# Performance work log

Hardware: AMD Instinct MI355X
Metric: run time of the kernel (lower is better)

## Reference

```python
import jax, jax.numpy as jnp
import numpy as np

B = 4096          # number of sampled constraints (batch)
H = 1024          # hidden_size
N_UNIT = 5
MAXD = 4          # max(DEPTHS)
TAU = 1.0
N_STEPS = N_UNIT * (1 + 2 * MAXD)  # 45
CLIST = np.linspace(10.0, 20.0, 5).astype(np.float32)
NSC = 11
DEPTH_VALS = np.array([2, 3, 4])
RATIO_VALS = np.array([3, 4, 6])
KS_VALS = np.array([3, 5, 7])


def setup_inputs() -> dict:
    key = jax.random.key(0)
    ks = jax.random.split(key, 20)
    def p(k, shape):
        return jax.random.uniform(k, shape, minval=-0.1, maxval=0.1, dtype=jnp.float32)
    return {
        'constraints': jax.random.uniform(ks[0], (B,), minval=10.0, maxval=20.0, dtype=jnp.float32),
        'superclass_id': 3,
        'gumbel_u': jax.random.uniform(ks[1], (N_STEPS, B, 3), minval=1e-6, maxval=1.0 - 1e-6, dtype=jnp.float32),
        'cond_emb': p(ks[2], (len(CLIST), H // 2)),
        'sc_emb': p(ks[3], (NSC, H // 2)),
        'depth_emb': p(ks[4], (3, H)),
        'ratio_emb': p(ks[5], (3, H)),
        'ks_emb': p(ks[6], (3, H)),
        'W_ih': p(ks[7], (4 * H, H)), 'b_ih': p(ks[8], (4 * H,)),
        'W_hh': p(ks[9], (4 * H, H)), 'b_hh': p(ks[10], (4 * H,)),
        'depth_W': p(ks[11], (3, H)), 'depth_b': p(ks[12], (3,)),
        'width_W': p(ks[13], (3, H)), 'width_b': p(ks[14], (3,)),
        'ks_W': p(ks[15], (3, H)), 'ks_b': p(ks[16], (3,)),
    }


def reference(constraints, superclass_id, gumbel_u, cond_emb, sc_emb, depth_emb, ratio_emb,
              ks_emb, W_ih, b_ih, W_hh, b_hh, depth_W, depth_b, width_W, width_b, ks_W, ks_b):
    clist = jnp.asarray(CLIST)
    # linear_interpolation: find bracketing interval for each constraint
    idx = jnp.clip(jnp.searchsorted(clist, constraints, side='right') - 1, 0, clist.shape[0] - 2)
    left, right = clist[idx], clist[idx + 1]
    w = ((right - constraints) / (right - left))[:, None]
    cemb = w * cond_emb[idx] + (1.0 - w) * cond_emb[idx + 1]          # [B, H/2]
    sce = jnp.broadcast_to(sc_emb[superclass_id], (constraints.shape[0], sc_emb.shape[1]))
    embed = jnp.concatenate([cemb, sce], axis=1)                       # [B, H]
    h = jnp.zeros((constraints.shape[0], H), embed.dtype)
    c = h

    def lstm(x, h, c):
        gates = x @ W_ih.T + b_ih + h @ W_hh.T + b_hh                  # [B, 4H]
        i, f, g, o = jnp.split(gates, 4, axis=-1)
        c2 = jax.nn.sigmoid(f) * c + jax.nn.sigmoid(i) * jnp.tanh(g)
        h2 = jax.nn.sigmoid(o) * jnp.tanh(c2)
        return h2, c2

    def gsample(logits, u):
        g = -jnp.log(-jnp.log(u))
        y_soft = jax.nn.softmax((logits + g) / TAU, axis=-1)
        onehot = jax.nn.one_hot(jnp.argmax(y_soft, -1), logits.shape[-1], dtype=y_soft.dtype)
        y_hard = onehot - jax.lax.stop_gradient(y_soft) + y_soft       # straight-through
        return jnp.argmax(y_hard, -1), y_soft, y_hard

    t = 0
    d_idx, d_probs, d_wbs = [], [], []
    r_idx, r_probs, r_wbs = [], [], []
    k_idx, k_probs, k_wbs = [], [], []
    for _unit in range(N_UNIT):
        h, c = lstm(embed, h, c)
        s, ys, yh = gsample(h @ depth_W.T + depth_b, gumbel_u[t]); t += 1
        d_idx.append(s); d_probs.append(ys); d_wbs.append(yh)
        embed = depth_emb[s]
        for _blk in range(MAXD):
            h, c = lstm(embed, h, c)
            s, ys, yh = gsample(h @ width_W.T + width_b, gumbel_u[t]); t += 1
            r_idx.append(s); r_probs.append(ys); r_wbs.append(yh)
            embed = ratio_emb[s]
            h, c = lstm(embed, h, c)
            s, ys, yh = gsample(h @ ks_W.T + ks_b, gumbel_u[t]); t += 1
            k_idx.append(s); k_probs.append(ys); k_wbs.append(yh)
            embed = ks_emb[s]

    depths = jnp.asarray(DEPTH_VALS)[jnp.stack(d_idx)]   # [5, B]
    ratios = jnp.asarray(RATIO_VALS)[jnp.stack(r_idx)]   # [20, B]
    kss = jnp.asarray(KS_VALS)[jnp.stack(k_idx)]         # [20, B]
    return (depths, ratios, kss,
            jnp.stack(d_wbs), jnp.stack(d_probs),
            jnp.stack(r_wbs), jnp.stack(r_probs),
            jnp.stack(k_wbs), jnp.stack(k_probs))
```

## Files before the change

kernel.cpp:

```cpp
#include <hip/hip_runtime.h>
#include <cmath>

namespace {

typedef _Float16 f16;
typedef f16 f16x8 __attribute__((ext_vector_type(8)));
typedef f16 f16x4 __attribute__((ext_vector_type(4)));
typedef float f32x4 __attribute__((ext_vector_type(4)));

constexpr int B  = 4096;
constexpr int H  = 1024;
constexpr int FH = 4 * H;
constexpr int NSTEPS = 45;
constexpr float INVS = 1.0f / 2048.0f;

__device__ __forceinline__ float sigf(float x) { return 1.0f / (1.0f + expf(-x)); }

struct HL { f16 h, l; };
__device__ __forceinline__ HL split16(float a) {
  float ah = (float)(f16)a;
  if (fabsf(a) < 6.1035156e-5f) ah = 0.0f;
  HL r; r.h = (f16)ah; r.l = (f16)((a - ah) * 2048.0f); return r;
}

__device__ __forceinline__ void async16(f16* lds_dst, const f16* gsrc) {
  __builtin_amdgcn_global_load_lds(
      (const __attribute__((address_space(1))) void*)gsrc,
      (__attribute__((address_space(3))) void*)lds_dst, 16, 0, 0);
}

__global__ void convertW_kernel(const float* __restrict__ W,
                                f16* __restrict__ Whi, f16* __restrict__ Wlo) {
  size_t i = ((size_t)blockIdx.x * 256 + threadIdx.x) * 4;
  float4 v = *(const float4*)(W + i);
  HL a = split16(v.x), b = split16(v.y), c = split16(v.z), d = split16(v.w);
  f16x4 hi = {a.h, b.h, c.h, d.h};
  f16x4 lo = {a.l, b.l, c.l, d.l};
  *(f16x4*)(Whi + i) = hi;
  *(f16x4*)(Wlo + i) = lo;
}

__global__ void precompute_kernel(
    const float* __restrict__ W_ih, const float* __restrict__ b_ih, const float* __restrict__ b_hh,
    const float* __restrict__ depth_emb, const float* __restrict__ ratio_emb, const float* __restrict__ ks_emb,
    const float* __restrict__ cond_emb, const float* __restrict__ sc_emb, const int* __restrict__ sid_p,
    float* __restrict__ tblD, float* __restrict__ tblR, float* __restrict__ tblK,
    float* __restrict__ condp, float* __restrict__ base0) {
  const int w4   = threadIdx.x >> 6;
  const int lane = threadIdx.x & 63;
  const int j    = blockIdx.x * 4 + w4;
  const float* wr = W_ih + (size_t)j * H;
  const int k = lane * 16;
  float4 wv0 = *(const float4*)(wr + k);
  float4 wv1 = *(const float4*)(wr + k + 4);
  float4 wv2 = *(const float4*)(wr + k + 8);
  float4 wv3 = *(const float4*)(wr + k + 12);

  auto dot = [&](const float* e) -> float {
    float4 e0 = *(const float4*)(e);
    float4 e1 = *(const float4*)(e + 4);
    float4 e2 = *(const float4*)(e + 8);
    float4 e3 = *(const float4*)(e + 12);
    return e0.x*wv0.x + e0.y*wv0.y + e0.z*wv0.z + e0.w*wv0.w
         + e1.x*wv1.x + e1.y*wv1.y + e1.z*wv1.z + e1.w*wv1.w
         + e2.x*wv2.x + e2.y*wv2.y + e2.z*wv2.z + e2.w*wv2.w
         + e3.x*wv3.x + e3.y*wv3.y + e3.z*wv3.z + e3.w*wv3.w;
  };

  float a[15];
  a[0] = dot(depth_emb + k);       a[1] = dot(depth_emb + H + k);   a[2] = dot(depth_emb + 2*H + k);
  a[3] = dot(ratio_emb + k);       a[4] = dot(ratio_emb + H + k);   a[5] = dot(ratio_emb + 2*H + k);
  a[6] = dot(ks_emb + k);          a[7] = dot(ks_emb + H + k);      a[8] = dot(ks_emb + 2*H + k);
  a[9] = a[10] = a[11] = a[12] = a[13] = a[14] = 0.0f;
  constexpr int HH = H / 2;
  int sid = sid_p[0];
  if (lane < 32) {
    a[9]  = dot(cond_emb + 0*HH + k);
    a[10] = dot(cond_emb + 1*HH + k);
    a[11] = dot(cond_emb + 2*HH + k);
    a[12] = dot(cond_emb + 3*HH + k);
    a[13] = dot(cond_emb + 4*HH + k);
  } else {
    a[14] = dot(sc_emb + sid*HH + (k - HH));
  }
  #pragma unroll
  for (int i = 0; i < 15; ++i) {
    #pragma unroll
    for (int off = 32; off > 0; off >>= 1) a[i] += __shfl_xor(a[i], off);
  }
  if (lane == 0) {
    float bias = b_ih[j] + b_hh[j];
    tblD[0*FH+j]=a[0]+bias; tblD[1*FH+j]=a[1]+bias; tblD[2*FH+j]=a[2]+bias;
    tblR[0*FH+j]=a[3]+bias; tblR[1*FH+j]=a[4]+bias; tblR[2*FH+j]=a[5]+bias;
    tblK[0*FH+j]=a[6]+bias; tblK[1*FH+j]=a[7]+bias; tblK[2*FH+j]=a[8]+bias;
    condp[0*FH+j]=a[9]; condp[1*FH+j]=a[10]; condp[2*FH+j]=a[11];
    condp[3*FH+j]=a[12]; condp[4*FH+j]=a[13];
    base0[j] = a[14] + bias;
  }
}

__global__ void step0_kernel(const float* __restrict__ constraints,
                             const float* __restrict__ condp, const float* __restrict__ base0,
                             f16* __restrict__ hhi, f16* __restrict__ hlo, float* __restrict__ c) {
  int idx = blockIdx.x * blockDim.x + threadIdx.x;
  int b = idx >> 10;
  int j = idx & (H - 1);
  float cv = constraints[b];
  int i0 = 0;
  if (cv >= 12.5f) i0 = 1;
  if (cv >= 15.0f) i0 = 2;
  if (cv >= 17.5f) i0 = 3;
  float right = 10.0f + 2.5f * (float)(i0 + 1);
  float w = (right - cv) / 2.5f;
  const float* c0 = condp + (size_t)i0 * FH;
  const float* c1 = c0 + FH;
  float iw = 1.0f - w;
  float xi = w*c0[j]       + iw*c1[j]       + base0[j];
  float xg = w*c0[2*H+j]   + iw*c1[2*H+j]   + base0[2*H+j];
  float xo = w*c0[3*H+j]   + iw*c1[3*H+j]   + base0[3*H+j];
  float cn = sigf(xi) * tanhf(xg);
  float hn = sigf(xo) * tanhf(cn);
  c[idx] = cn;
  HL s = split16(hn);
  hhi[idx] = s.h; hlo[idx] = s.l;
}

constexpr int BUFE = 24576;

__global__ __launch_bounds__(512, 2) void lstm_step_mfma(
    const f16* __restrict__ hhi, const f16* __restrict__ hlo,
    f16* __restrict__ nhhi, f16* __restrict__ nhlo,
    float* __restrict__ cbuf,
    const f16* __restrict__ Whi, const f16* __restrict__ Wlo,
    const float* __restrict__ tbl, const int* __restrict__ sel) {
  __shared__ __align__(16) f16 lds[3 * BUFE];

  const int tid  = threadIdx.x;
  const int lane = tid & 63;
  const int w    = tid >> 6;
  const int wm   = w >> 1, wn = w & 1;
  const int l15  = lane & 15;
  const int kq   = lane >> 4;

  const int L   = blockIdx.x;
  const int xcd = L & 7, seq = L >> 3;
  const int jb  = (xcd << 2) + (seq & 3);
  const int bb  = seq >> 2;
  const int b0  = bb << 8;
  const int j0  = jb << 5;

  f32x4 accH[4][4] = {};
  f32x4 accL[4][4] = {};

  int offA[4], offB[4];
  #pragma unroll
  for (int mf = 0; mf < 4; ++mf) {
    int R = wm * 64 + mf * 16 + l15;
    int c = kq ^ (R & 3) ^ ((R >> 2) & 3);
    offA[mf] = R * 32 + c * 8;
  }
  #pragma unroll
  for (int nf = 0; nf < 4; ++nf) {
    int R = nf * 32 + wn * 16 + l15;
    int c = kq ^ (R & 3) ^ ((R >> 2) & 3);
    offB[nf] = 16384 + R * 32 + c * 8;
  }

  const int rs = tid >> 2, cs = tid & 3;
  const int r1 = 128 + rs;
  const int cl0 = cs ^ (rs & 3) ^ ((rs >> 2) & 3);
  const int cl1 = cs ^ (r1 & 3) ^ ((r1 >> 2) & 3);
  const int wrow = ((rs >> 5) << 10) + j0 + (rs & 31);
  const f16* sA0h = hhi + (size_t)(b0 + rs) * H + cl0 * 8;
  const f16* sA0l = hlo + (size_t)(b0 + rs) * H + cl0 * 8;
  const f16* sA1h = hhi + (size_t)(b0 + r1) * H + cl1 * 8;
  const f16* sA1l = hlo + (size_t)(b0 + r1) * H + cl1 * 8;
  const f16* sBh  = Whi + (size_t)wrow * H + cl0 * 8;
  const f16* sBl  = Wlo + (size_t)wrow * H + cl0 * 8;
  const int dA0 = w * 512, dA1 = 4096 + w * 512, dB = 16384 + w * 512;

  auto stage6 = [&](f16* buf, int ko) {
    async16(buf + dA0,        sA0h + ko);
    async16(buf + dA0 + 8192, sA0l + ko);
    async16(buf + dA1,        sA1h + ko);
    async16(buf + dA1 + 8192, sA1l + ko);
    async16(buf + dB,         sBh + ko);
    async16(buf + dB + 4096,  sBl + ko);
  };

  f16 *bA = lds, *bB = lds + BUFE, *bC = lds + 2 * BUFE;

  f16x8 bhX[4], bhY[4];

  stage6(bA, 0);
  stage6(bB, 32);
  asm volatile("s_waitcnt vmcnt(0)" ::: "memory");
  __builtin_amdgcn_s_barrier();
  #pragma unroll
  for (int nf = 0; nf < 4; ++nf) bhX[nf] = *(const f16x8*)(bA + offB[nf]);

  auto tile = [&](int kt, f16x8 (&bhC)[4], f16x8 (&bhN)[4]) {
    if (kt < 30) stage6(bC, (kt + 2) * 32);

    f16x8 ah[4], al[4], bl[4];
    #pragma unroll
    for (int mf = 0; mf < 4; ++mf) ah[mf] = *(const f16x8*)(bA + offA[mf]);
    #pragma unroll
    for (int mf = 0; mf < 4; ++mf) al[mf] = *(const f16x8*)(bA + offA[mf] + 8192);
    #pragma unroll
    for (int nf = 0; nf < 4; ++nf) bl[nf] = *(const f16x8*)(bA + offB[nf] + 4096);
    if (kt < 31) {
      #pragma unroll
      for (int nf = 0; nf < 4; ++nf) bhN[nf] = *(const f16x8*)(bB + offB[nf]);
    }

    #pragma unroll
    for (int mf = 0; mf < 4; ++mf)
      #pragma unroll
      for (int nf = 0; nf < 4; ++nf)
        accH[mf][nf] = __builtin_amdgcn_mfma_f32_16x16x32_f16(ah[mf], bhC[nf], accH[mf][nf], 0, 0, 0);
    #pragma unroll
    for (int mf = 0; mf < 4; ++mf)
      #pragma unroll
      for (int nf = 0; nf < 4; ++nf)
        accL[mf][nf] = __builtin_amdgcn_mfma_f32_16x16x32_f16(ah[mf], bl[nf], accL[mf][nf], 0, 0, 0);
    #pragma unroll
    for (int mf = 0; mf < 4; ++mf)
      #pragma unroll
      for (int nf = 0; nf < 4; ++nf)
        accL[mf][nf] = __builtin_amdgcn_mfma_f32_16x16x32_f16(al[mf], bhC[nf], accL[mf][nf], 0, 0, 0);

    asm volatile("s_waitcnt vmcnt(0)" ::: "memory");
    __builtin_amdgcn_s_barrier();
    f16* t = bA; bA = bB; bB = bC; bC = t;
  };

  for (int kt = 0; kt < 32; kt += 2) {
    tile(kt,     bhX, bhY);
    tile(kt + 1, bhY, bhX);
  }

  const int j = j0 + wn * 16 + l15;
  #pragma unroll
  for (int mf = 0; mf < 4; ++mf) {
    #pragma unroll
    for (int r = 0; r < 4; ++r) {
      int b = b0 + wm * 64 + mf * 16 + kq * 4 + r;
      int s = sel[b];
      const float* tb = tbl + (size_t)s * FH + j;
      float gi = accH[mf][0][r] + accL[mf][0][r] * INVS + tb[0];
      float gf = accH[mf][1][r] + accL[mf][1][r] * INVS + tb[H];
      float gg = accH[mf][2][r] + accL[mf][2][r] * INVS + tb[2*H];
      float go = accH[mf][3][r] + accL[mf][3][r] * INVS + tb[3*H];
      size_t off = (size_t)b * H + j;
      float cp = cbuf[off];
      float cn = sigf(gf) * cp + sigf(gi) * tanhf(gg);
      float hn = sigf(go) * tanhf(cn);
      cbuf[off] = cn;
      HL sp = split16(hn);
      nhhi[off] = sp.h;
      nhlo[off] = sp.l;
    }
  }
}

__global__ void sampler_kernel(const f16* __restrict__ hhi, const f16* __restrict__ hlo,
                               const float* __restrict__ selW, const float* __restrict__ selb,
                               const float* __restrict__ gu,
                               float* __restrict__ val_out, float* __restrict__ wb_out,
                               float* __restrict__ p_out,
                               float v0, float v1, float v2,
                               int* __restrict__ sel) {
  int wave = threadIdx.x >> 6;
  int lane = threadIdx.x & 63;
  int b = blockIdx.x * 4 + wave;
  const f16* hh = hhi + (size_t)b * H;
  const f16* hl = hlo + (size_t)b * H;
  float acc0 = 0, acc1 = 0, acc2 = 0;
  #pragma unroll
  for (int ch = 0; ch < 4; ++ch) {
    int k = ch * 256 + lane * 4;
    f16x4 vh = *(const f16x4*)(hh + k);
    f16x4 vl = *(const f16x4*)(hl + k);
    float x0 = (float)vh[0] + (float)vl[0] * INVS;
    float x1 = (float)vh[1] + (float)vl[1] * INVS;
    float x2 = (float)vh[2] + (float)vl[2] * INVS;
    float x3 = (float)vh[3] + (float)vl[3] * INVS;
    float4 w0 = *(const float4*)(selW + k);
    float4 w1 = *(const float4*)(selW + H + k);
    float4 w2 = *(const float4*)(selW + 2*H + k);
    acc0 += x0*w0.x + x1*w0.y + x2*w0.z + x3*w0.w;
    acc1 += x0*w1.x + x1*w1.y + x2*w1.z + x3*w1.w;
    acc2 += x0*w2.x + x1*w2.y + x2*w2.z + x3*w2.w;
  }
  #pragma unroll
  for (int off = 32; off > 0; off >>= 1) {
    acc0 += __shfl_xor(acc0, off);
    acc1 += __shfl_xor(acc1, off);
    acc2 += __shfl_xor(acc2, off);
  }
  if (lane == 0) {
    float y0 = acc0 + selb[0] - logf(-logf(gu[(size_t)b*3 + 0]));
    float y1 = acc1 + selb[1] - logf(-logf(gu[(size_t)b*3 + 1]));
    float y2 = acc2 + selb[2] - logf(-logf(gu[(size_t)b*3 + 2]));
    int s = 0;
    float best = y0;
    if (y1 > best) { s = 1; best = y1; }
    if (y2 > best) { s = 2; best = y2; }
    float e0 = expf(y0 - best), e1 = expf(y1 - best), e2 = expf(y2 - best);
    float inv = 1.0f / (e0 + e1 + e2);
    float p0 = e0 * inv, p1 = e1 * inv, p2 = e2 * inv;
    val_out[b] = (s == 0) ? v0 : ((s == 1) ? v1 : v2);
    wb_out[(size_t)b*3 + 0] = (s == 0) ? 1.0f : 0.0f;
    wb_out[(size_t)b*3 + 1] = (s == 1) ? 1.0f : 0.0f;
    wb_out[(size_t)b*3 + 2] = (s == 2) ? 1.0f : 0.0f;
    p_out[(size_t)b*3 + 0] = p0;
    p_out[(size_t)b*3 + 1] = p1;
    p_out[(size_t)b*3 + 2] = p2;
    sel[b] = s;
  }
}

}

extern "C" void kernel_launch(void* const* d_in, const int* in_sizes, int n_in,
                              void* d_out, int out_size, void* d_ws, size_t ws_size,
                              hipStream_t stream) {
  (void)in_sizes; (void)n_in; (void)out_size; (void)ws_size;
  const float* constraints = (const float*)d_in[0];
  const int*   sid         = (const int*)d_in[1];
  const float* gumbel      = (const float*)d_in[2];
  const float* cond_emb    = (const float*)d_in[3];
  const float* sc_emb      = (const float*)d_in[4];
  const float* depth_emb   = (const float*)d_in[5];
  const float* ratio_emb   = (const float*)d_in[6];
  const float* ks_emb      = (const float*)d_in[7];
  const float* W_ih        = (const float*)d_in[8];
  const float* b_ih        = (const float*)d_in[9];
  const float* W_hh        = (const float*)d_in[10];
  const float* b_hh        = (const float*)d_in[11];
  const float* depth_W     = (const float*)d_in[12];
  const float* depth_b     = (const float*)d_in[13];
  const float* width_W     = (const float*)d_in[14];
  const float* width_b     = (const float*)d_in[15];
  const float* ks_W        = (const float*)d_in[16];
  const float* ks_b        = (const float*)d_in[17];

  float* out = (float*)d_out;
  float* ws  = (float*)d_ws;

  float* cb    = ws;
  f16*   W16hi = (f16*)(cb + (size_t)B * H);
  f16*   W16lo = W16hi + (size_t)FH * H;
  f16*   hhiA  = W16lo + (size_t)FH * H;
  f16*   hloA  = hhiA + (size_t)B * H;
  f16*   hhiB  = hloA + (size_t)B * H;
  f16*   hloB  = hhiB + (size_t)B * H;
  float* tblD  = (float*)(hloB + (size_t)B * H);
  float* tblR  = tblD + 3 * FH;
  float* tblK  = tblR + 3 * FH;
  float* condp = tblK + 3 * FH;
  float* base0 = condp + 5 * FH;
  int*   sel   = (int*)(base0 + FH);

  convertW_kernel<<<(FH * H / 4) / 256, 256, 0, stream>>>(W_hh, W16hi, W16lo);
  precompute_kernel<<<FH / 4, 256, 0, stream>>>(
      W_ih, b_ih, b_hh, depth_emb, ratio_emb, ks_emb, cond_emb, sc_emb, sid,
      tblD, tblR, tblK, condp, base0);
  step0_kernel<<<(B * H) / 256, 256, 0, stream>>>(constraints, condp, base0, hhiA, hloA, cb);

  const float* selW_arr[3] = {depth_W, width_W, ks_W};
  const float* selb_arr[3] = {depth_b, width_b, ks_b};
  const float vals[3][3]   = {{2.f,3.f,4.f},{3.f,4.f,6.f},{3.f,5.f,7.f}};
  float* tbl_arr[3]        = {tblD, tblR, tblK};

  const size_t DEPTHS = 0,            RATIOS = (size_t)5*B,   KSS    = (size_t)25*B,
               DWBS   = (size_t)45*B, DPROBS = (size_t)60*B,
               RWBS   = (size_t)75*B, RPROBS = (size_t)135*B,
               KWBS   = (size_t)195*B, KPROBS = (size_t)255*B;

  f16* hhi_cur = hhiA; f16* hlo_cur = hloA;
  f16* hhi_nxt = hhiB; f16* hlo_nxt = hloB;
  for (int t = 0; t < NSTEPS; ++t) {
    if (t > 0) {
      int pt = (t - 1) % 9;
      int ptype = (pt == 0) ? 0 : ((pt & 1) ? 1 : 2);
      lstm_step_mfma<<<512, 512, 0, stream>>>(
          hhi_cur, hlo_cur, hhi_nxt, hlo_nxt, cb, W16hi, W16lo, tbl_arr[ptype], sel);
      f16* th = hhi_cur; hhi_cur = hhi_nxt; hhi_nxt = th;
      f16* tl = hlo_cur; hlo_cur = hlo_nxt; hlo_nxt = tl;
    }
    int r = t % 9, u = t / 9;
    int ty, row;
    float *valp, *wbp, *pp;
    if (r == 0)      { ty = 0; row = u;
      valp = out + DEPTHS + (size_t)row*B; wbp = out + DWBS + (size_t)row*B*3; pp = out + DPROBS + (size_t)row*B*3; }
    else if (r & 1)  { ty = 1; row = u*4 + (r-1)/2;
      valp = out + RATIOS + (size_t)row*B; wbp = out + RWBS + (size_t)row*B*3; pp = out + RPROBS + (size_t)row*B*3; }
    else             { ty = 2; row = u*4 + (r-2)/2;
      valp = out + KSS + (size_t)row*B;    wbp = out + KWBS + (size_t)row*B*3; pp = out + KPROBS + (size_t)row*B*3; }
    sampler_kernel<<<B / 4, 256, 0, stream>>>(
        hhi_cur, hlo_cur, selW_arr[ty], selb_arr[ty], gumbel + (size_t)t * B * 3,
        valp, wbp, pp, vals[ty][0], vals[ty][1], vals[ty][2], sel);
  }
}
```

Measured before the change: 5.367 ms.

## Interleave LDS loads, async prefetch and MFMA in ping-pong phases with priority

Restructures the K-loop of the LSTM gate GEMM into four phases per tile. Each phase loads one B fragment, issues part of the next-next tile's async copies, and runs its MFMAs under raised wave priority, with barriers in between. Waiting on vmcnt(6) instead of vmcnt(0) keeps one tile's prefetch in flight across iterations, and the B register double-buffering is dropped. The aim is better overlap of memory and matrix work, at the cost of extra barriers per tile and reliance on exact vmcnt counting for correctness.

New measurement: 5.508 ms. 2.6% more time.

```diff
diff --git a/kernel.cpp b/kernel.cpp
--- a/kernel.cpp
+++ b/kernel.cpp
@@ -190,54 +190,52 @@
 
   f16 *bA = lds, *bB = lds + BUFE, *bC = lds + 2 * BUFE;
 
-  f16x8 bhX[4], bhY[4];
-
   stage6(bA, 0);
   stage6(bB, 32);
-  asm volatile("s_waitcnt vmcnt(0)" ::: "memory");
+  asm volatile("s_waitcnt vmcnt(6)" ::: "memory");
   __builtin_amdgcn_s_barrier();
-  #pragma unroll
-  for (int nf = 0; nf < 4; ++nf) bhX[nf] = *(const f16x8*)(bA + offB[nf]);
-
-  auto tile = [&](int kt, f16x8 (&bhC)[4], f16x8 (&bhN)[4]) {
-    if (kt < 30) stage6(bC, (kt + 2) * 32);
-
-    f16x8 ah[4], al[4], bl[4];
+
+  for (int kt = 0; kt < 32; ++kt) {
+    const int ko2 = (kt + 2) * 32;
+    const bool pre = (kt < 30);
+    f16x8 ah[4], al[4];
+
     #pragma unroll
-    for (int mf = 0; mf < 4; ++mf) ah[mf] = *(const f16x8*)(bA + offA[mf]);
-    #pragma unroll
-    for (int mf = 0; mf < 4; ++mf) al[mf] = *(const f16x8*)(bA + offA[mf] + 8192);
-    #pragma unroll
-    for (int nf = 0; nf < 4; ++nf) bl[nf] = *(const f16x8*)(bA + offB[nf] + 4096);
-    if (kt < 31) {
+    for (int nf = 0; nf < 4; ++nf) {
+      if (nf == 0) {
+        #pragma unroll
+        for (int mf = 0; mf < 4; ++mf) ah[mf] = *(const f16x8*)(bA + offA[mf]);
+        #pragma unroll
+        for (int mf = 0; mf < 4; ++mf) al[mf] = *(const f16x8*)(bA + offA[mf] + 8192);
+      }
+      f16x8 bh = *(const f16x8*)(bA + offB[nf]);
+      f16x8 bl = *(const f16x8*)(bA + offB[nf] + 4096);
+      if (pre) {
+        if (nf == 0) { async16(bC + dA0, sA0h + ko2); async16(bC + dA0 + 8192, sA0l + ko2); }
+        if (nf == 1) { async16(bC + dA1, sA1h + ko2); async16(bC + dA1 + 8192, sA1l + ko2); }
+        if (nf == 2) { async16(bC + dB,  sBh + ko2);  async16(bC + dB + 4096,  sBl + ko2); }
+      }
+      __builtin_amdgcn_s_barrier();
+      asm volatile("s_waitcnt lgkmcnt(0)" ::: "memory");
+      __builtin_amdgcn_s_setprio(1);
       #pragma unroll
-      for (int nf = 0; nf < 4; ++nf) bhN[nf] = *(const f16x8*)(bB + offB[nf]);
+      for (int mf = 0; mf < 4; ++mf)
+        accH[mf][nf] = __builtin_amdgcn_mfma_f32_16x16x32_f16(ah[mf], bh, accH[mf][nf], 0, 0, 0);
+      #pragma unroll
+      for (int mf = 0; mf < 4; ++mf)
+        accL[mf][nf] = __builtin_amdgcn_mfma_f32_16x16x32_f16(ah[mf], bl, accL[mf][nf], 0, 0, 0);
+      #pragma unroll
+      for (int mf = 0; mf < 4; ++mf)
+        accL[mf][nf] = __builtin_amdgcn_mfma_f32_16x16x32_f16(al[mf], bh, accL[mf][nf], 0, 0, 0);
+      __builtin_amdgcn_s_setprio(0);
+      if (nf == 3) {
+        if (pre) asm volatile("s_waitcnt vmcnt(6)" ::: "memory");
+        else     asm volatile("s_waitcnt vmcnt(0)" ::: "memory");
+      }
+      __builtin_amdgcn_s_barrier();
     }
 
-    #pragma unroll
-    for (int mf = 0; mf < 4; ++mf)
-      #pragma unroll
-      for (int nf = 0; nf < 4; ++nf)
-        accH[mf][nf] = __builtin_amdgcn_mfma_f32_16x16x32_f16(ah[mf], bhC[nf], accH[mf][nf], 0, 0, 0);
-    #pragma unroll
-    for (int mf = 0; mf < 4; ++mf)
-      #pragma unroll
-      for (int nf = 0; nf < 4; ++nf)
-        accL[mf][nf] = __builtin_amdgcn_mfma_f32_16x16x32_f16(ah[mf], bl[nf], accL[mf][nf], 0, 0, 0);
-    #pragma unroll
-    for (int mf = 0; mf < 4; ++mf)
-      #pragma unroll
-      for (int nf = 0; nf < 4; ++nf)
-        accL[mf][nf] = __builtin_amdgcn_mfma_f32_16x16x32_f16(al[mf], bhC[nf], accL[mf][nf], 0, 0, 0);
-
-    asm volatile("s_waitcnt vmcnt(0)" ::: "memory");
-    __builtin_amdgcn_s_barrier();
     f16* t = bA; bA = bB; bB = bC; bC = t;
-  };
-
-  for (int kt = 0; kt < 32; kt += 2) {
-    tile(kt,     bhX, bhY);
-    tile(kt + 1, bhY, bhX);
   }
 
   const int j = j0 + wn * 16 + l15;
```
